# Performance work log

Measured on AMD Instinct MI355X. Metric: run time of the kernel, lower is better.

Reference implementation:

```python
import jax, jax.numpy as jnp
import numpy as np

D_MODEL = 512
N = 1024
BS = 64


def setup_inputs() -> dict:
    key = jax.random.key(0)
    ks = jax.random.split(key, 4)
    x = jax.random.normal(ks[0], (BS, N, D_MODEL), dtype=jnp.float32)
    # nn.Linear init per init_weights(): weight ~ N(0, 0.001), bias = 0
    Wq = 0.001 * jax.random.normal(ks[1], (D_MODEL, D_MODEL), dtype=jnp.float32)
    Wk = 0.001 * jax.random.normal(ks[2], (D_MODEL, D_MODEL), dtype=jnp.float32)
    Wv = 0.001 * jax.random.normal(ks[3], (D_MODEL, D_MODEL), dtype=jnp.float32)
    bq = jnp.zeros((D_MODEL,), dtype=jnp.float32)
    bk = jnp.zeros((D_MODEL,), dtype=jnp.float32)
    bv = jnp.zeros((D_MODEL,), dtype=jnp.float32)
    pos_bias = jnp.ones((N, N), dtype=jnp.float32)  # nn.Parameter(ones)
    return {"x": x, "Wq": Wq, "bq": bq, "Wk": Wk, "bk": bk,
            "Wv": Wv, "bv": bv, "pos_bias": pos_bias}


def reference(x, Wq, bq, Wk, bk, Wv, bv, pos_bias):
    # q,k,v: [bs, n, d] via Linear (y = x W^T + b)
    q = jnp.einsum('bnd,ed->bne', x, Wq) + bq
    k = jnp.einsum('bnd,ed->bne', x, Wk) + bk
    v = jnp.einsum('bnd,ed->bne', x, Wv) + bv
    # exp(k[b,j,d] + bias[i,j]) factorizes exactly: exp(bias) * exp(k).
    # This avoids the (n, bs, n, d) broadcast intermediate of the original
    # while computing identical math.
    ek = jnp.exp(k)                                   # [bs, n, d]
    eb = jnp.exp(pos_bias)                            # [n_i, n_j]
    numerator = jnp.einsum('ij,bjd->bid', eb, ek * v)  # sum over j
    denominator = jnp.einsum('ij,bjd->bid', eb, ek)
    out = jax.nn.sigmoid(q) * (numerator / denominator)  # [bs, n, d]
    return out
```

## Files before the change

### kernel.cpp

```cpp
#include <hip/hip_runtime.h>
#include <hip/hip_bf16.h>
#include <stdint.h>


#define NSEQ 1024
#define DM   512

typedef __attribute__((ext_vector_type(8))) short bf16x8;
typedef __attribute__((ext_vector_type(4))) float f32x4;

static __device__ __forceinline__ float b2f(unsigned short u) {
    union { uint32_t i; float f; } c; c.i = ((uint32_t)u) << 16; return c.f;
}
static __device__ __forceinline__ unsigned short f2b(float f) {
    union { float f; uint32_t i; } c; c.f = f;
    uint32_t r = c.i + 0x7FFFu + ((c.i >> 16) & 1u);
    return (unsigned short)(r >> 16);
}
static __device__ __forceinline__ void gl_lds16(const unsigned short* g, unsigned short* l) {
    __builtin_amdgcn_global_load_lds(
        (const __attribute__((address_space(1))) unsigned int*)(g),
        (__attribute__((address_space(3))) unsigned int*)(l), 16, 0, 0);
}

#define PH_BAR() do { asm volatile("" ::: "memory"); \
    __builtin_amdgcn_s_barrier(); asm volatile("" ::: "memory"); } while (0)

__global__ void k_flag0(unsigned int* flag) { *flag = 0u; }

__global__ void k_flag(const float* __restrict__ pb, unsigned int* __restrict__ flag) {
    int i = blockIdx.x * 256 + threadIdx.x;
    float4 v = reinterpret_cast<const float4*>(pb)[i];
    float p0 = pb[0];
    if (v.x != p0 || v.y != p0 || v.z != p0 || v.w != p0) atomicOr(flag, 1u);
}

__global__ void k_eb(const float* __restrict__ pb, unsigned short* __restrict__ eb,
                     const unsigned int* __restrict__ flag) {
    if (*flag == 0u) return;
    int i = blockIdx.x * 256 + threadIdx.x;
    float4 v = reinterpret_cast<const float4*>(pb)[i];
    union { unsigned short u[4]; uint2 p; } o;
    o.u[0] = f2b(__expf(v.x)); o.u[1] = f2b(__expf(v.y));
    o.u[2] = f2b(__expf(v.z)); o.u[3] = f2b(__expf(v.w));
    reinterpret_cast<uint2*>(eb)[i] = o.p;
}

__global__ void k_cvt(const float* __restrict__ src, unsigned short* __restrict__ dst) {
    int i = blockIdx.x * 256 + threadIdx.x;
    const float4* p = reinterpret_cast<const float4*>(src) + (size_t)i * 2;
    float4 f0 = p[0], f1 = p[1];
    union { unsigned short u[8]; int4 v; } o;
    o.u[0]=f2b(f0.x); o.u[1]=f2b(f0.y); o.u[2]=f2b(f0.z); o.u[3]=f2b(f0.w);
    o.u[4]=f2b(f1.x); o.u[5]=f2b(f1.y); o.u[6]=f2b(f1.z); o.u[7]=f2b(f1.w);
    reinterpret_cast<int4*>(dst)[i] = o.v;
}

__global__ void k_cvt_kv(const float* __restrict__ src, unsigned short* __restrict__ Wb,
                         int toff) {
    int i = blockIdx.x * 256 + threadIdx.x;
    int r = i >> 6, c8 = i & 63;
    const float4* p = reinterpret_cast<const float4*>(src + (size_t)r * DM + c8 * 8);
    float4 f0 = p[0], f1 = p[1];
    union { unsigned short u[8]; int4 v; } o;
    o.u[0]=f2b(f0.x); o.u[1]=f2b(f0.y); o.u[2]=f2b(f0.z); o.u[3]=f2b(f0.w);
    o.u[4]=f2b(f1.x); o.u[5]=f2b(f1.y); o.u[6]=f2b(f1.z); o.u[7]=f2b(f1.w);
    int r2 = 512 + ((r >> 7) << 8) + ((r & 127) << 1) + toff;
    *reinterpret_cast<int4*>(&Wb[(size_t)r2 * DM + c8 * 8]) = o.v;
}

template<int NT>
static __device__ __forceinline__ void gemm_p(
    const unsigned short* __restrict__ Abase,
    const unsigned short* __restrict__ Bbase,
    int lda, int ldb, unsigned short* smem, f32x4 (&acc)[8][4],
    int wave, int lane)
{
    const int wr = wave >> 2, wq = wave & 3;
    const int lrow = lane & 15, lkg = lane >> 4;
    const int po  = lane >> 3;
    const int sub = (lane >> 2) & 1;
    const int qp  = lane & 3;

    auto stage = [&](int mat, int s, int h, int t) {
        int p = h * 64 + wave * 8 + po;
        int r = p * 2 + sub;
        int q = qp ^ (p & 3);
        int col = ((t & (NT - 1)) << 5) + q * 8;
        const unsigned short* g = (mat ? Bbase + (size_t)r * ldb
                                       : Abase + (size_t)r * lda) + col;
        unsigned short* d = smem + mat * 32768 + s * 8192 + (h * 64 + wave * 8) * 64;
        gl_lds16(g, d);
    };
    auto loadA = [&](int s, int h, bf16x8* af) {
        const unsigned short* base = smem + s * 8192;
        #pragma unroll
        for (int mi = 0; mi < 4; ++mi) {
            int r = wr * 128 + h * 64 + mi * 16 + lrow;
            int p = r >> 1;
            af[mi] = *reinterpret_cast<const bf16x8*>(
                base + p * 64 + (r & 1) * 32 + ((lkg ^ (p & 3)) << 3));
        }
    };
    auto loadB = [&](int s, bf16x8* bf) {
        const unsigned short* base = smem + 32768 + s * 8192;
        #pragma unroll
        for (int ni = 0; ni < 4; ++ni) {
            int r = wq * 64 + ni * 16 + lrow;
            int p = r >> 1;
            bf[ni] = *reinterpret_cast<const bf16x8*>(
                base + p * 64 + (r & 1) * 32 + ((lkg ^ (p & 3)) << 3));
        }
    };
    auto mfma16 = [&](int h, bf16x8* af, bf16x8* bf) {
        __builtin_amdgcn_s_setprio(1);
        #pragma unroll
        for (int mi = 0; mi < 4; ++mi)
            #pragma unroll
            for (int ni = 0; ni < 4; ++ni)
                acc[h * 4 + mi][ni] = __builtin_amdgcn_mfma_f32_16x16x32_bf16(
                    af[mi], bf[ni], acc[h * 4 + mi][ni], 0, 0, 0);
        __builtin_amdgcn_s_setprio(0);
    };

    #pragma unroll
    for (int pt = 0; pt < 3; ++pt) {
        stage(0, pt, 0, pt); stage(0, pt, 1, pt);
        stage(1, pt, 0, pt); stage(1, pt, 1, pt);
    }
    asm volatile("s_waitcnt vmcnt(8)" ::: "memory");
    __builtin_amdgcn_s_barrier();

    #pragma unroll 1
    for (int tt = 0; tt < NT; tt += 4) {
        #pragma unroll
        for (int u = 0; u < 4; ++u) {
            const int t = tt + u;
            const int s = u, s3 = (u + 3) & 3, t3 = t + 3;
            bf16x8 af[4], bfr[4];
            loadB(s, bfr); loadA(s, 0, af);
            stage(0, s3, 0, t3); stage(0, s3, 1, t3);
            mfma16(0, af, bfr);
            loadA(s, 1, af);
            stage(1, s3, 0, t3); stage(1, s3, 1, t3);
            mfma16(1, af, bfr);
            asm volatile("s_waitcnt vmcnt(8)" ::: "memory");
            __builtin_amdgcn_s_barrier();
        }
    }
    asm volatile("s_waitcnt vmcnt(0)" ::: "memory");
    __builtin_amdgcn_s_barrier();
}

__launch_bounds__(512)
__global__ void k_kv(const unsigned short* __restrict__ xb,
                     const unsigned short* __restrict__ Wb,
                     const float* __restrict__ bk, const float* __restrict__ bv,
                     unsigned short* __restrict__ Z,
                     float* __restrict__ P,
                     const unsigned int* __restrict__ flag)
{
    extern __shared__ unsigned short smem[];
    const int bid = blockIdx.x;
    const int logical = (bid & 7) * 128 + (bid >> 3);
    const int mtile = logical >> 2, e4 = logical & 3;
    const int brow = mtile * 256;
    const int b = brow >> 10, jtile = (brow >> 8) & 3;
    const bool uni = (*flag == 0u);

    const int tid = threadIdx.x;
    const int lane = tid & 63, wave = tid >> 6;
    const int wr = wave >> 2, wq = wave & 3;
    const int lrow = lane & 15, lkg = lane >> 4;

    f32x4 acc[8][4];
    const f32x4 z4 = {0.f, 0.f, 0.f, 0.f};
    #pragma unroll
    for (int a = 0; a < 8; ++a)
        #pragma unroll
        for (int c = 0; c < 4; ++c) acc[a][c] = z4;

    gemm_p<16>(xb + (size_t)brow * DM, Wb + (size_t)(512 + e4 * 256) * DM, DM, DM,
               smem, acc, wave, lane);

    if (uni) {
        const int sub = lane & 1;
        float* SF = reinterpret_cast<float*>(smem);
        float se[4], sv2[4];
        #pragma unroll
        for (int ni = 0; ni < 4; ++ni) {
            int n = wq * 64 + ni * 16 + lrow;
            int d = e4 * 128 + (n >> 1);
            float bia = sub ? bv[d] : bk[d];
            float accv = 0.f, acce = 0.f;
            #pragma unroll
            for (int mi = 0; mi < 8; ++mi) {
                #pragma unroll
                for (int r = 0; r < 4; ++r) {
                    float val = acc[mi][ni][r] + bia;
                    float e = sub ? val : __expf(val);
                    float partner = __shfl_xor(e, 1);
                    if (!sub) { accv += e * partner; acce += e; }
                }
            }
            accv += __shfl_xor(accv, 16); accv += __shfl_xor(accv, 32);
            acce += __shfl_xor(acce, 16); acce += __shfl_xor(acce, 32);
            se[ni] = acce; sv2[ni] = accv;
        }
        __syncthreads();
        if (sub == 0 && lkg == 0) {
            #pragma unroll
            for (int ni = 0; ni < 4; ++ni) {
                int dl = wq * 32 + ni * 8 + (lrow >> 1);
                SF[wr * 256 + dl * 2]     = sv2[ni];
                SF[wr * 256 + dl * 2 + 1] = se[ni];
            }
        }
        __syncthreads();
        if (tid < 128) {
            int dl = tid, d = e4 * 128 + dl;
            float num = SF[dl * 2]     + SF[256 + dl * 2];
            float den = SF[dl * 2 + 1] + SF[256 + dl * 2 + 1];
            P[b * 2048 + jtile * 512 + d] = num;
            P[131072 + b * 2048 + jtile * 512 + d] = den;
        }
    } else {
        unsigned short* T = smem;
        #pragma unroll
        for (int pp = 0; pp < 2; ++pp) {
            __syncthreads();
            if (wr == pp) {
                #pragma unroll
                for (int mi = 0; mi < 8; ++mi) {
                    int m0 = mi*16 + lkg*4;
                    #pragma unroll
                    for (int ni = 0; ni < 4; ++ni) {
                        int n = wq*64 + ni*16 + lrow;
                        int sub = n & 1;
                        int d = e4 * 128 + (n >> 1);
                        float bia = sub ? bv[d] : bk[d];
                        union { unsigned short u[4]; uint2 p; } o;
                        #pragma unroll
                        for (int r = 0; r < 4; ++r) {
                            float tv = acc[mi][ni][r] + bia;
                            o.u[r] = f2b(sub ? tv : __expf(tv));
                        }
                        *reinterpret_cast<uint2*>(&T[n * 136 + m0]) = o.p;
                    }
                }
            }
            __syncthreads();
            const int j0 = (brow & (NSEQ - 1)) + pp * 128;
            #pragma unroll
            for (int it = 0; it < 8; ++it) {
                int idx = it * 512 + tid;
                int zr = idx >> 4, jg = idx & 15;
                int t = zr >> 7, dli = zr & 127;
                int d = e4 * 128 + dli;
                union { unsigned short u[8]; int4 v; } o;
                if (t == 0) {
                    union { unsigned short u[8]; int4 v; } pe, pv;
                    pe.v = *reinterpret_cast<const int4*>(&T[(2*dli)     * 136 + jg*8]);
                    pv.v = *reinterpret_cast<const int4*>(&T[(2*dli + 1) * 136 + jg*8]);
                    #pragma unroll
                    for (int j = 0; j < 8; ++j) o.u[j] = f2b(b2f(pe.u[j]) * b2f(pv.u[j]));
                } else {
                    o.v = *reinterpret_cast<const int4*>(&T[(2*dli) * 136 + jg*8]);
                }
                int nz = ((d >> 4) << 5) + t * 16 + (d & 15);
                size_t off = ((size_t)(b * NSEQ + nz)) * NSEQ + j0 + jg * 8;
                *reinterpret_cast<int4*>(&Z[off]) = o.v;
            }
        }
    }
}

__launch_bounds__(256)
__global__ void k_sum2(const float* __restrict__ P,
                       const unsigned int* __restrict__ flag,
                       float* __restrict__ R)
{
    if (*flag != 0u) return;
    int gid = blockIdx.x * 256 + threadIdx.x;
    int b = gid >> 9, d = gid & 511;
    const float* p0 = P + b * 2048 + d;
    const float* p1 = P + 131072 + b * 2048 + d;
    float num = p0[0] + p0[512] + p0[1024] + p0[1536];
    float den = p1[0] + p1[512] + p1[1024] + p1[1536];
    R[gid] = num / den;
}

__launch_bounds__(512)
__global__ void k_q(const unsigned short* __restrict__ xb,
                    const unsigned short* __restrict__ Wb,
                    const float* __restrict__ bq,
                    const float* __restrict__ R,
                    unsigned short* __restrict__ s_out,
                    float* __restrict__ out,
                    const unsigned int* __restrict__ flag)
{
    extern __shared__ unsigned short smem[];
    const int bid = blockIdx.x;
    const int logical = (bid & 7) * 256 + (bid >> 3);
    const int mtile = logical >> 2, etile = logical & 3;
    const int brow = mtile * 128;
    const int ecol = etile * 128;
    const int b = brow >> 10;
    const bool uni = (*flag == 0u);

    const int tid = threadIdx.x;
    const int lane = tid & 63, wave = tid >> 6;
    const int wr = wave >> 2, wq = wave & 3;
    const int lrow = lane & 15, lkg = lane >> 4;
    const int po = lane >> 3, sub = (lane >> 2) & 1, qp = lane & 3;

    const unsigned short* Abase = xb + (size_t)brow * DM;
    const unsigned short* Bbase = Wb + (size_t)ecol * DM;

    f32x4 acc[4][2];
    const f32x4 z4 = {0.f, 0.f, 0.f, 0.f};
    #pragma unroll
    for (int a = 0; a < 4; ++a)
        #pragma unroll
        for (int c = 0; c < 2; ++c) acc[a][c] = z4;

    auto stg = [&](int mat, int s, int t) {
        int p = wave * 8 + po;
        int r = p * 2 + sub;
        int q = qp ^ (p & 3);
        int col = (t << 5) + q * 8;
        const unsigned short* g = (mat ? Bbase + (size_t)r * DM
                                       : Abase + (size_t)r * DM) + col;
        gl_lds16(g, smem + mat * 8192 + s * 4096 + (wave * 8) * 64);
    };
    auto ldA = [&](int s, bf16x8* af) {
        const unsigned short* base = smem + s * 4096;
        #pragma unroll
        for (int mi = 0; mi < 4; ++mi) {
            int r = wr * 64 + mi * 16 + lrow, p = r >> 1;
            af[mi] = *reinterpret_cast<const bf16x8*>(
                base + p * 64 + (r & 1) * 32 + ((lkg ^ (p & 3)) << 3));
        }
    };
    auto ldB = [&](int s, bf16x8* bf) {
        const unsigned short* base = smem + 8192 + s * 4096;
        #pragma unroll
        for (int ni = 0; ni < 2; ++ni) {
            int r = wq * 32 + ni * 16 + lrow, p = r >> 1;
            bf[ni] = *reinterpret_cast<const bf16x8*>(
                base + p * 64 + (r & 1) * 32 + ((lkg ^ (p & 3)) << 3));
        }
    };

    stg(0, 0, 0); stg(1, 0, 0);
    asm volatile("s_waitcnt vmcnt(0)" ::: "memory");
    __builtin_amdgcn_s_barrier();

    #pragma unroll 1
    for (int tt = 0; tt < 16; tt += 2) {
        #pragma unroll
        for (int u = 0; u < 2; ++u) {
            const int t = tt + u;
            const int s = u, sn = u ^ 1;
            if (t + 1 < 16) { stg(0, sn, t + 1); stg(1, sn, t + 1); }
            bf16x8 af[4], bf[2];
            ldB(s, bf); ldA(s, af);
            __builtin_amdgcn_s_setprio(1);
            #pragma unroll
            for (int mi = 0; mi < 4; ++mi)
                #pragma unroll
                for (int ni = 0; ni < 2; ++ni)
                    acc[mi][ni] = __builtin_amdgcn_mfma_f32_16x16x32_bf16(
                        af[mi], bf[ni], acc[mi][ni], 0, 0, 0);
            __builtin_amdgcn_s_setprio(0);
            asm volatile("s_waitcnt vmcnt(0)" ::: "memory");
            __builtin_amdgcn_s_barrier();
        }
    }

    unsigned short* T = smem;
    #pragma unroll
    for (int mi = 0; mi < 4; ++mi) {
        int m0 = wr * 64 + mi * 16 + lkg * 4;
        #pragma unroll
        for (int ni = 0; ni < 2; ++ni) {
            int nl = wq * 32 + ni * 16 + lrow;
            float bia = bq[ecol + nl];
            #pragma unroll
            for (int r = 0; r < 4; ++r) {
                float tq = acc[mi][ni][r] + bia;
                float sg = __builtin_amdgcn_rcpf(1.f + __expf(-tq));
                T[(m0 + r) * 136 + nl] = f2b(sg);
            }
        }
    }
    __syncthreads();
    if (uni) {
        #pragma unroll
        for (int it = 0; it < 4; ++it) {
            int idx = it * 512 + tid;
            int m = idx >> 4, ng = idx & 15;
            union { unsigned short u[8]; int4 v; } sv;
            sv.v = *reinterpret_cast<const int4*>(&T[m * 136 + ng * 8]);
            int dcol = ecol + ng * 8;
            const float4* rp = reinterpret_cast<const float4*>(&R[b * 512 + dcol]);
            float4 r0 = rp[0], r1 = rp[1];
            float4 o0, o1;
            o0.x = b2f(sv.u[0]) * r0.x; o0.y = b2f(sv.u[1]) * r0.y;
            o0.z = b2f(sv.u[2]) * r0.z; o0.w = b2f(sv.u[3]) * r0.w;
            o1.x = b2f(sv.u[4]) * r1.x; o1.y = b2f(sv.u[5]) * r1.y;
            o1.z = b2f(sv.u[6]) * r1.z; o1.w = b2f(sv.u[7]) * r1.w;
            float4* op = reinterpret_cast<float4*>(&out[(size_t)(brow + m) * DM + dcol]);
            op[0] = o0; op[1] = o1;
        }
    } else {
        #pragma unroll
        for (int it = 0; it < 4; ++it) {
            int idx = it * 512 + tid;
            int m = idx >> 4, ng = idx & 15;
            int4 vv = *reinterpret_cast<const int4*>(&T[m * 136 + ng * 8]);
            *reinterpret_cast<int4*>(
                &s_out[(size_t)(brow + m) * DM + ecol + ng * 8]) = vv;
        }
    }
}

__launch_bounds__(512)
__global__ void k_aft(const unsigned short* __restrict__ eb,
                      const unsigned short* __restrict__ Z,
                      const unsigned short* __restrict__ s_in,
                      const unsigned int* __restrict__ flag,
                      float* __restrict__ out)
{
    if (*flag == 0u) return;
    extern __shared__ unsigned short smem[];
    const int bid = blockIdx.x;
    const int logical = (bid & 7) * 32 + (bid >> 3);
    const int itile = logical & 3, ncol = logical >> 2;
    const int i0 = itile * 256;

    const int tid = threadIdx.x;
    const int lane = tid & 63, wave = tid >> 6;
    const int wr = wave >> 2, wq = wave & 3;
    const int lrow = lane & 15, lkg = lane >> 4;
    const int po = lane >> 3, sub = (lane >> 2) & 1, qp = lane & 3;
    const int ch0 = wave * 2;

    const unsigned short* Abase = eb + (size_t)i0 * NSEQ;
    const unsigned short* Bbase = Z + (size_t)ncol * 4 * 256 * NSEQ;

    f32x4 acc[8][4];
    const f32x4 z4 = {0.f, 0.f, 0.f, 0.f};
    #pragma unroll
    for (int a = 0; a < 8; ++a)
        #pragma unroll
        for (int c = 0; c < 4; ++c) acc[a][c] = z4;

    auto half = [&](int isB, int d, int c) -> unsigned short* {
        return smem + isB * 32768 + (d * 2 + c) * 8192;
    };
    auto stg = [&](int isB, int d, int c, int t) {
        int ta = t & 63, gp = ta >> 4, tk = ta & 15;
        unsigned short* dst = half(isB, d, c);
        #pragma unroll
        for (int q2 = 0; q2 < 2; ++q2) {
            int ch = ch0 + q2;
            int p = ch * 8 + po, r = p * 2 + sub;
            int col = (tk << 6) + (c << 5) + ((qp ^ (p & 3)) << 3);
            const unsigned short* g = isB
                ? Bbase + ((size_t)(gp * 256 + r)) * NSEQ + col
                : Abase + (size_t)r * NSEQ + col;
            gl_lds16(g, dst + ch * 512);
        }
    };
    auto ldA = [&](int d, int c, int h, bf16x8* af) {
        const unsigned short* base = half(0, d, c);
        #pragma unroll
        for (int mi = 0; mi < 4; ++mi) {
            int r = wr * 128 + h * 64 + mi * 16 + lrow, p = r >> 1;
            af[mi] = *reinterpret_cast<const bf16x8*>(
                base + p * 64 + (r & 1) * 32 + ((lkg ^ (p & 3)) << 3));
        }
    };
    auto ldB = [&](int d, int c, bf16x8* bf) {
        const unsigned short* base = half(1, d, c);
        #pragma unroll
        for (int ni = 0; ni < 4; ++ni) {
            int r = wq * 64 + ni * 16 + lrow, p = r >> 1;
            bf[ni] = *reinterpret_cast<const bf16x8*>(
                base + p * 64 + (r & 1) * 32 + ((lkg ^ (p & 3)) << 3));
        }
    };
    auto mm = [&](int h, bf16x8* af, bf16x8* bf) {
        __builtin_amdgcn_s_setprio(1);
        #pragma unroll
        for (int mi = 0; mi < 4; ++mi)
            #pragma unroll
            for (int ni = 0; ni < 4; ++ni)
                acc[h * 4 + mi][ni] = __builtin_amdgcn_mfma_f32_16x16x32_bf16(
                    af[mi], bf[ni], acc[h * 4 + mi][ni], 0, 0, 0);
        __builtin_amdgcn_s_setprio(0);
    };

    stg(0, 0, 0, 0); stg(1, 0, 0, 0);
    stg(0, 0, 1, 0); stg(1, 0, 1, 0);
    stg(0, 1, 0, 1); stg(1, 1, 0, 1);
    asm volatile("s_waitcnt vmcnt(4)" ::: "memory");
    __builtin_amdgcn_s_barrier();
    asm volatile("" ::: "memory");

    #pragma unroll 1
    for (int g = 0; g < 4; ++g) {
        #pragma unroll 1
        for (int ii = 0; ii < 8; ++ii) {
            const int T = (g << 4) + (ii << 1);
            const int U = T + 1, T2 = T + 2, U2 = T + 3;
            bf16x8 af[4], bf[4];
            ldB(0, 0, bf); ldA(0, 0, 0, af); stg(0, 1, 1, U);
            PH_BAR(); mm(0, af, bf); PH_BAR();
            ldA(0, 0, 1, af); stg(1, 1, 1, U);
            PH_BAR(); mm(1, af, bf); PH_BAR();
            ldB(0, 1, bf); ldA(0, 1, 0, af); stg(0, 0, 0, T2);
            PH_BAR(); mm(0, af, bf); PH_BAR();
            ldA(0, 1, 1, af); stg(1, 0, 0, T2);
            asm volatile("s_waitcnt vmcnt(4)" ::: "memory");
            PH_BAR(); mm(1, af, bf); PH_BAR();
            ldB(1, 0, bf); ldA(1, 0, 0, af); stg(0, 0, 1, T2);
            PH_BAR(); mm(0, af, bf); PH_BAR();
            ldA(1, 0, 1, af); stg(1, 0, 1, T2);
            PH_BAR(); mm(1, af, bf); PH_BAR();
            ldB(1, 1, bf); ldA(1, 1, 0, af); stg(0, 1, 0, U2);
            PH_BAR(); mm(0, af, bf); PH_BAR();
            ldA(1, 1, 1, af); stg(1, 1, 0, U2);
            asm volatile("s_waitcnt vmcnt(4)" ::: "memory");
            PH_BAR(); mm(1, af, bf); PH_BAR();
        }
        const int n0 = (ncol * 4 + g) * 256;
        #pragma unroll
        for (int mi = 0; mi < 8; ++mi) {
            int i = i0 + wr*128 + mi*16 + lkg*4;
            #pragma unroll
            for (int pi = 0; pi < 2; ++pi) {
                int nA = n0 + wq*64 + pi*32 + lrow;
                int b  = nA >> 10, nn = nA & (NSEQ - 1);
                int d  = ((nn >> 5) << 4) + (nn & 15);
                #pragma unroll
                for (int r = 0; r < 4; ++r) {
                    size_t o = ((size_t)(b * NSEQ + i + r)) * DM + d;
                    out[o] = b2f(s_in[o]) * acc[mi][pi*2][r] / acc[mi][pi*2 + 1][r];
                }
                acc[mi][pi*2] = z4; acc[mi][pi*2 + 1] = z4;
            }
        }
    }
    asm volatile("s_waitcnt vmcnt(0)" ::: "memory");
}

extern "C" void kernel_launch(void* const* d_in, const int* in_sizes, int n_in,
                              void* d_out, int out_size, void* d_ws, size_t ws_size,
                              hipStream_t stream)
{
    const float* x  = (const float*)d_in[0];
    const float* Wq = (const float*)d_in[1];
    const float* bq = (const float*)d_in[2];
    const float* Wk = (const float*)d_in[3];
    const float* bk = (const float*)d_in[4];
    const float* Wv = (const float*)d_in[5];
    const float* bv = (const float*)d_in[6];
    const float* pb = (const float*)d_in[7];
    float* out = (float*)d_out;

    char* ws = (char*)d_ws;
    unsigned short* eb   = (unsigned short*)(ws);
    float*          Pbuf = (float*)(ws);
    unsigned short* Wb   = (unsigned short*)(ws + ((size_t)2 << 20));
    unsigned int*   flag = (unsigned int*)(ws + 0x380000);
    float*          Rbuf = (float*)(ws + 0x384000);
    unsigned short* xb   = (unsigned short*)(ws + ((size_t)4   << 20));
    unsigned short* s    = (unsigned short*)(ws + ((size_t)68  << 20));
    unsigned short* Z    = (unsigned short*)(ws + ((size_t)132 << 20));

    k_flag0<<<1, 1, 0, stream>>>(flag);
    k_flag<<<1024, 256, 0, stream>>>(pb, flag);
    k_eb <<<1024, 256, 0, stream>>>(pb, eb, flag);
    k_cvt<<<16384, 256, 0, stream>>>(x,  xb);
    k_cvt<<<128,   256, 0, stream>>>(Wq, Wb);
    k_cvt_kv<<<128, 256, 0, stream>>>(Wk, Wb, 0);
    k_cvt_kv<<<128, 256, 0, stream>>>(Wv, Wb, 1);
    k_kv<<<1024, 512, 131072, stream>>>(xb, Wb, bk, bv, Z, Pbuf, flag);
    k_sum2<<<128, 256, 0, stream>>>(Pbuf, flag, Rbuf);
    k_q<<<2048, 512, 34816, stream>>>(xb, Wb, bq, Rbuf, s, out, flag);
    k_aft<<<256, 512, 131072, stream>>>(eb, Z, s, flag, out);
}
```

Baseline: 196.3 us.

## Fuse fp32-to-bf16 conversion of x into the KV and Q GEMM A-loads

Removes the separate k_cvt pass over x. The KV and Q GEMMs now read fp32 x directly into registers, convert it to bf16, and write it into LDS. The KV GEMM pipeline shrinks from a 4-stage async global-to-LDS pipeline to 2-stage double buffering with __syncthreads, which cuts LDS use. The trade-off is that x is read as fp32 twice (by k_kv and k_q), doubling A-operand bytes, and A loads now pass through registers instead of async LDS loads, which weakens latency hiding.

```diff
diff --git a/kernel.cpp b/kernel.cpp
--- a/kernel.cpp
+++ b/kernel.cpp
@@ -69,91 +69,8 @@
     *reinterpret_cast<int4*>(&Wb[(size_t)r2 * DM + c8 * 8]) = o.v;
 }
 
-template<int NT>
-static __device__ __forceinline__ void gemm_p(
-    const unsigned short* __restrict__ Abase,
-    const unsigned short* __restrict__ Bbase,
-    int lda, int ldb, unsigned short* smem, f32x4 (&acc)[8][4],
-    int wave, int lane)
-{
-    const int wr = wave >> 2, wq = wave & 3;
-    const int lrow = lane & 15, lkg = lane >> 4;
-    const int po  = lane >> 3;
-    const int sub = (lane >> 2) & 1;
-    const int qp  = lane & 3;
-
-    auto stage = [&](int mat, int s, int h, int t) {
-        int p = h * 64 + wave * 8 + po;
-        int r = p * 2 + sub;
-        int q = qp ^ (p & 3);
-        int col = ((t & (NT - 1)) << 5) + q * 8;
-        const unsigned short* g = (mat ? Bbase + (size_t)r * ldb
-                                       : Abase + (size_t)r * lda) + col;
-        unsigned short* d = smem + mat * 32768 + s * 8192 + (h * 64 + wave * 8) * 64;
-        gl_lds16(g, d);
-    };
-    auto loadA = [&](int s, int h, bf16x8* af) {
-        const unsigned short* base = smem + s * 8192;
-        #pragma unroll
-        for (int mi = 0; mi < 4; ++mi) {
-            int r = wr * 128 + h * 64 + mi * 16 + lrow;
-            int p = r >> 1;
-            af[mi] = *reinterpret_cast<const bf16x8*>(
-                base + p * 64 + (r & 1) * 32 + ((lkg ^ (p & 3)) << 3));
-        }
-    };
-    auto loadB = [&](int s, bf16x8* bf) {
-        const unsigned short* base = smem + 32768 + s * 8192;
-        #pragma unroll
-        for (int ni = 0; ni < 4; ++ni) {
-            int r = wq * 64 + ni * 16 + lrow;
-            int p = r >> 1;
-            bf[ni] = *reinterpret_cast<const bf16x8*>(
-                base + p * 64 + (r & 1) * 32 + ((lkg ^ (p & 3)) << 3));
-        }
-    };
-    auto mfma16 = [&](int h, bf16x8* af, bf16x8* bf) {
-        __builtin_amdgcn_s_setprio(1);
-        #pragma unroll
-        for (int mi = 0; mi < 4; ++mi)
-            #pragma unroll
-            for (int ni = 0; ni < 4; ++ni)
-                acc[h * 4 + mi][ni] = __builtin_amdgcn_mfma_f32_16x16x32_bf16(
-                    af[mi], bf[ni], acc[h * 4 + mi][ni], 0, 0, 0);
-        __builtin_amdgcn_s_setprio(0);
-    };
-
-    #pragma unroll
-    for (int pt = 0; pt < 3; ++pt) {
-        stage(0, pt, 0, pt); stage(0, pt, 1, pt);
-        stage(1, pt, 0, pt); stage(1, pt, 1, pt);
-    }
-    asm volatile("s_waitcnt vmcnt(8)" ::: "memory");
-    __builtin_amdgcn_s_barrier();
-
-    #pragma unroll 1
-    for (int tt = 0; tt < NT; tt += 4) {
-        #pragma unroll
-        for (int u = 0; u < 4; ++u) {
-            const int t = tt + u;
-            const int s = u, s3 = (u + 3) & 3, t3 = t + 3;
-            bf16x8 af[4], bfr[4];
-            loadB(s, bfr); loadA(s, 0, af);
-            stage(0, s3, 0, t3); stage(0, s3, 1, t3);
-            mfma16(0, af, bfr);
-            loadA(s, 1, af);
-            stage(1, s3, 0, t3); stage(1, s3, 1, t3);
-            mfma16(1, af, bfr);
-            asm volatile("s_waitcnt vmcnt(8)" ::: "memory");
-            __builtin_amdgcn_s_barrier();
-        }
-    }
-    asm volatile("s_waitcnt vmcnt(0)" ::: "memory");
-    __builtin_amdgcn_s_barrier();
-}
-
 __launch_bounds__(512)
-__global__ void k_kv(const unsigned short* __restrict__ xb,
+__global__ void k_kv(const float* __restrict__ x,
                      const unsigned short* __restrict__ Wb,
                      const float* __restrict__ bk, const float* __restrict__ bv,
                      unsigned short* __restrict__ Z,
@@ -172,6 +89,10 @@
     const int lane = tid & 63, wave = tid >> 6;
     const int wr = wave >> 2, wq = wave & 3;
     const int lrow = lane & 15, lkg = lane >> 4;
+    const int po = lane >> 3, sub0 = (lane >> 2) & 1, qp = lane & 3;
+
+    const float* Ax = x + (size_t)brow * DM;
+    const unsigned short* Bb = Wb + (size_t)(512 + e4 * 256) * DM;
 
     f32x4 acc[8][4];
     const f32x4 z4 = {0.f, 0.f, 0.f, 0.f};
@@ -180,8 +101,80 @@
         #pragma unroll
         for (int c = 0; c < 4; ++c) acc[a][c] = z4;
 
-    gemm_p<16>(xb + (size_t)brow * DM, Wb + (size_t)(512 + e4 * 256) * DM, DM, DM,
-               smem, acc, wave, lane);
+    auto stgB = [&](int s, int h, int t) {
+        int p = h * 64 + wave * 8 + po;
+        int r = p * 2 + sub0;
+        int col = (t << 5) + ((qp ^ (p & 3)) << 3);
+        gl_lds16(Bb + (size_t)r * DM + col,
+                 smem + 16384 + s * 8192 + (h * 64 + wave * 8) * 64);
+    };
+    auto ldAreg = [&](int t, int h, float4* f) {
+        int p = h * 64 + wave * 8 + po;
+        int r = p * 2 + sub0;
+        int col = (t << 5) + ((qp ^ (p & 3)) << 3);
+        const float4* sp = reinterpret_cast<const float4*>(Ax + (size_t)r * DM + col);
+        f[0] = sp[0]; f[1] = sp[1];
+    };
+    auto wrA = [&](int s, int h, const float4* f) {
+        union { unsigned short u[8]; int4 v; } o;
+        o.u[0]=f2b(f[0].x); o.u[1]=f2b(f[0].y); o.u[2]=f2b(f[0].z); o.u[3]=f2b(f[0].w);
+        o.u[4]=f2b(f[1].x); o.u[5]=f2b(f[1].y); o.u[6]=f2b(f[1].z); o.u[7]=f2b(f[1].w);
+        *reinterpret_cast<int4*>(
+            smem + s * 8192 + (h * 64 + wave * 8) * 64 + lane * 8) = o.v;
+    };
+    auto ldAf = [&](int s, int h, bf16x8* af) {
+        const unsigned short* base = smem + s * 8192;
+        #pragma unroll
+        for (int mi = 0; mi < 4; ++mi) {
+            int r = wr * 128 + h * 64 + mi * 16 + lrow, p = r >> 1;
+            af[mi] = *reinterpret_cast<const bf16x8*>(
+                base + p * 64 + (r & 1) * 32 + ((lkg ^ (p & 3)) << 3));
+        }
+    };
+    auto ldBf = [&](int s, bf16x8* bf) {
+        const unsigned short* base = smem + 16384 + s * 8192;
+        #pragma unroll
+        for (int ni = 0; ni < 4; ++ni) {
+            int r = wq * 64 + ni * 16 + lrow, p = r >> 1;
+            bf[ni] = *reinterpret_cast<const bf16x8*>(
+                base + p * 64 + (r & 1) * 32 + ((lkg ^ (p & 3)) << 3));
+        }
+    };
+    auto mfma16 = [&](int h, bf16x8* af, bf16x8* bf) {
+        __builtin_amdgcn_s_setprio(1);
+        #pragma unroll
+        for (int mi = 0; mi < 4; ++mi)
+            #pragma unroll
+            for (int ni = 0; ni < 4; ++ni)
+                acc[h * 4 + mi][ni] = __builtin_amdgcn_mfma_f32_16x16x32_bf16(
+                    af[mi], bf[ni], acc[h * 4 + mi][ni], 0, 0, 0);
+        __builtin_amdgcn_s_setprio(0);
+    };
+
+    {
+        float4 fA0[2], fA1[2];
+        ldAreg(0, 0, fA0); ldAreg(0, 1, fA1);
+        stgB(0, 0, 0); stgB(0, 1, 0);
+        wrA(0, 0, fA0); wrA(0, 1, fA1);
+        __syncthreads();
+    }
+    #pragma unroll 1
+    for (int t = 0; t < 16; ++t) {
+        const int s = t & 1, sn = s ^ 1;
+        const bool more = (t + 1 < 16);
+        float4 fN0[2], fN1[2];
+        if (more) {
+            ldAreg(t + 1, 0, fN0); ldAreg(t + 1, 1, fN1);
+            stgB(sn, 0, t + 1); stgB(sn, 1, t + 1);
+        }
+        bf16x8 af[4], bfr[4];
+        ldBf(s, bfr); ldAf(s, 0, af);
+        mfma16(0, af, bfr);
+        ldAf(s, 1, af);
+        mfma16(1, af, bfr);
+        if (more) { wrA(sn, 0, fN0); wrA(sn, 1, fN1); }
+        __syncthreads();
+    }
 
     if (uni) {
         const int sub = lane & 1;
@@ -291,7 +284,7 @@
 }
 
 __launch_bounds__(512)
-__global__ void k_q(const unsigned short* __restrict__ xb,
+__global__ void k_q(const float* __restrict__ x,
                     const unsigned short* __restrict__ Wb,
                     const float* __restrict__ bq,
                     const float* __restrict__ R,
@@ -312,10 +305,10 @@
     const int lane = tid & 63, wave = tid >> 6;
     const int wr = wave >> 2, wq = wave & 3;
     const int lrow = lane & 15, lkg = lane >> 4;
-    const int po = lane >> 3, sub = (lane >> 2) & 1, qp = lane & 3;
-
-    const unsigned short* Abase = xb + (size_t)brow * DM;
-    const unsigned short* Bbase = Wb + (size_t)ecol * DM;
+    const int po = lane >> 3, sub0 = (lane >> 2) & 1, qp = lane & 3;
+
+    const float* Ax = x + (size_t)brow * DM;
+    const unsigned short* Bb = Wb + (size_t)ecol * DM;
 
     f32x4 acc[4][2];
     const f32x4 z4 = {0.f, 0.f, 0.f, 0.f};
@@ -324,16 +317,28 @@
         #pragma unroll
         for (int c = 0; c < 2; ++c) acc[a][c] = z4;
 
-    auto stg = [&](int mat, int s, int t) {
+    auto stgB = [&](int s, int t) {
         int p = wave * 8 + po;
-        int r = p * 2 + sub;
-        int q = qp ^ (p & 3);
-        int col = (t << 5) + q * 8;
-        const unsigned short* g = (mat ? Bbase + (size_t)r * DM
-                                       : Abase + (size_t)r * DM) + col;
-        gl_lds16(g, smem + mat * 8192 + s * 4096 + (wave * 8) * 64);
-    };
-    auto ldA = [&](int s, bf16x8* af) {
+        int r = p * 2 + sub0;
+        int col = (t << 5) + ((qp ^ (p & 3)) << 3);
+        gl_lds16(Bb + (size_t)r * DM + col,
+                 smem + 8192 + s * 4096 + (wave * 8) * 64);
+    };
+    auto ldAreg = [&](int t, float4* f) {
+        int p = wave * 8 + po;
+        int r = p * 2 + sub0;
+        int col = (t << 5) + ((qp ^ (p & 3)) << 3);
+        const float4* sp = reinterpret_cast<const float4*>(Ax + (size_t)r * DM + col);
+        f[0] = sp[0]; f[1] = sp[1];
+    };
+    auto wrA = [&](int s, const float4* f) {
+        union { unsigned short u[8]; int4 v; } o;
+        o.u[0]=f2b(f[0].x); o.u[1]=f2b(f[0].y); o.u[2]=f2b(f[0].z); o.u[3]=f2b(f[0].w);
+        o.u[4]=f2b(f[1].x); o.u[5]=f2b(f[1].y); o.u[6]=f2b(f[1].z); o.u[7]=f2b(f[1].w);
+        *reinterpret_cast<int4*>(
+            smem + s * 4096 + (wave * 8) * 64 + lane * 8) = o.v;
+    };
+    auto ldAf = [&](int s, bf16x8* af) {
         const unsigned short* base = smem + s * 4096;
         #pragma unroll
         for (int mi = 0; mi < 4; ++mi) {
@@ -342,7 +347,7 @@
                 base + p * 64 + (r & 1) * 32 + ((lkg ^ (p & 3)) << 3));
         }
     };
-    auto ldB = [&](int s, bf16x8* bf) {
+    auto ldBf = [&](int s, bf16x8* bf) {
         const unsigned short* base = smem + 8192 + s * 4096;
         #pragma unroll
         for (int ni = 0; ni < 2; ++ni) {
@@ -352,30 +357,31 @@
         }
     };
 
-    stg(0, 0, 0); stg(1, 0, 0);
-    asm volatile("s_waitcnt vmcnt(0)" ::: "memory");
-    __builtin_amdgcn_s_barrier();
-
+    {
+        float4 fA[2];
+        ldAreg(0, fA);
+        stgB(0, 0);
+        wrA(0, fA);
+        __syncthreads();
+    }
     #pragma unroll 1
-    for (int tt = 0; tt < 16; tt += 2) {
-        #pragma unroll
-        for (int u = 0; u < 2; ++u) {
-            const int t = tt + u;
-            const int s = u, sn = u ^ 1;
-            if (t + 1 < 16) { stg(0, sn, t + 1); stg(1, sn, t + 1); }
-            bf16x8 af[4], bf[2];
-            ldB(s, bf); ldA(s, af);
-            __builtin_amdgcn_s_setprio(1);
-            #pragma unroll
-            for (int mi = 0; mi < 4; ++mi)
-                #pragma unroll
-                for (int ni = 0; ni < 2; ++ni)
-                    acc[mi][ni] = __builtin_amdgcn_mfma_f32_16x16x32_bf16(
-                        af[mi], bf[ni], acc[mi][ni], 0, 0, 0);
-            __builtin_amdgcn_s_setprio(0);
-            asm volatile("s_waitcnt vmcnt(0)" ::: "memory");
-            __builtin_amdgcn_s_barrier();
-        }
+    for (int t = 0; t < 16; ++t) {
+        const int s = t & 1, sn = s ^ 1;
+        const bool more = (t + 1 < 16);
+        float4 fN[2];
+        if (more) { ldAreg(t + 1, fN); stgB(sn, t + 1); }
+        bf16x8 af[4], bf[2];
+        ldBf(s, bf); ldAf(s, af);
+        __builtin_amdgcn_s_setprio(1);
+        #pragma unroll
+        for (int mi = 0; mi < 4; ++mi)
+            #pragma unroll
+            for (int ni = 0; ni < 2; ++ni)
+                acc[mi][ni] = __builtin_amdgcn_mfma_f32_16x16x32_bf16(
+                    af[mi], bf[ni], acc[mi][ni], 0, 0, 0);
+        __builtin_amdgcn_s_setprio(0);
+        if (more) wrA(sn, fN);
+        __syncthreads();
     }
 
     unsigned short* T = smem;
@@ -576,19 +582,17 @@
     unsigned short* Wb   = (unsigned short*)(ws + ((size_t)2 << 20));
     unsigned int*   flag = (unsigned int*)(ws + 0x380000);
     float*          Rbuf = (float*)(ws + 0x384000);
-    unsigned short* xb   = (unsigned short*)(ws + ((size_t)4   << 20));
     unsigned short* s    = (unsigned short*)(ws + ((size_t)68  << 20));
     unsigned short* Z    = (unsigned short*)(ws + ((size_t)132 << 20));
 
     k_flag0<<<1, 1, 0, stream>>>(flag);
     k_flag<<<1024, 256, 0, stream>>>(pb, flag);
     k_eb <<<1024, 256, 0, stream>>>(pb, eb, flag);
-    k_cvt<<<16384, 256, 0, stream>>>(x,  xb);
     k_cvt<<<128,   256, 0, stream>>>(Wq, Wb);
     k_cvt_kv<<<128, 256, 0, stream>>>(Wk, Wb, 0);
     k_cvt_kv<<<128, 256, 0, stream>>>(Wv, Wb, 1);
-    k_kv<<<1024, 512, 131072, stream>>>(xb, Wb, bk, bv, Z, Pbuf, flag);
+    k_kv<<<1024, 512, 69632, stream>>>(x, Wb, bk, bv, Z, Pbuf, flag);
     k_sum2<<<128, 256, 0, stream>>>(Pbuf, flag, Rbuf);
-    k_q<<<2048, 512, 34816, stream>>>(xb, Wb, bq, Rbuf, s, out, flag);
+    k_q<<<2048, 512, 34816, stream>>>(x, Wb, bq, Rbuf, s, out, flag);
     k_aft<<<256, 512, 131072, stream>>>(eb, Z, s, flag, out);
 }
```

After: 189.8 us, median of 2. 1.03x faster.
